# Kernel tuning notes

Hardware: AMD Instinct MI355X
Metric: run time of the kernel (lower is better)

Reference implementation:

```python
import jax, jax.numpy as jnp
import numpy as np

F_REP = 256
F_BET = 512
N_PER = 6
MAGNITUDE = 0.001


def _glorot(key, shape):
    fan_in = shape[0]
    return jax.random.normal(key, shape, dtype=jnp.float32) / np.sqrt(fan_in)


def setup_inputs() -> dict:
    key = jax.random.key(0)
    ks = jax.random.split(key, 24)
    n_atoms, n_tors = 50000, 300000
    inp = {
        'h': jax.random.normal(ks[0], (n_atoms, F_REP), dtype=jnp.float32),
        'idxs': jax.random.randint(ks[1], (n_tors, 4), 0, n_atoms, dtype=jnp.int64),
        # symmetrizer: skippedLinear(4*rep, bet) + DenseBlock(bet, depth=3)
        'Ws0': _glorot(ks[2], (4 * F_REP, F_BET)), 'bs0': jnp.zeros((F_BET,), jnp.float32),
        'Ws1': _glorot(ks[3], (F_BET, F_BET)), 'bs1': jnp.zeros((F_BET,), jnp.float32),
        'Ws2': _glorot(ks[4], (F_BET, F_BET)), 'bs2': jnp.zeros((F_BET,), jnp.float32),
        'Ws3': _glorot(ks[5], (F_BET, F_BET)), 'bs3': jnp.zeros((F_BET,), jnp.float32),
        # torsion_nn: DenseBlock(bet, depth=2) + Linear(bet, n_periodicity)
        'Wt0': _glorot(ks[6], (F_BET, F_BET)), 'bt0': jnp.zeros((F_BET,), jnp.float32),
        'Wt1': _glorot(ks[7], (F_BET, F_BET)), 'bt1': jnp.zeros((F_BET,), jnp.float32),
        'Wt2': _glorot(ks[8], (F_BET, N_PER)), 'bt2': jnp.zeros((N_PER,), jnp.float32),
        # classification_nn: skippedLinear(bet, bet) + Linear(bet, n_periodicity)
        'Wc0': _glorot(ks[9], (F_BET, F_BET)), 'bc0': jnp.zeros((F_BET,), jnp.float32),
        'Wc1': _glorot(ks[10], (F_BET, N_PER)), 'bc1': jnp.zeros((N_PER,), jnp.float32),
    }
    return inp


def _symmetrizer(x, Ws0, bs0, Ws1, bs1, Ws2, bs2, Ws3, bs3):
    # skippedLinear(4*rep, bet): dims differ -> plain Linear + ELU
    h = jax.nn.elu(x @ Ws0 + bs0)
    # DenseBlock: residual Linear+ELU layers (in==out)
    for W, b in ((Ws1, bs1), (Ws2, bs2), (Ws3, bs3)):
        h = h + jax.nn.elu(h @ W + b)
    return h


def reference(h, idxs, Ws0, bs0, Ws1, bs1, Ws2, bs2, Ws3, bs3,
              Wt0, bt0, Wt1, bt1, Wt2, bt2, Wc0, bc0, Wc1, bc1):
    feats = h[idxs]  # [N, 4, F_REP] gather
    f1, f2, f3, f4 = feats[:, 0], feats[:, 1], feats[:, 2], feats[:, 3]
    x_fwd = jnp.concatenate([f1, f2, f3, f4], axis=-1)  # [N, 4F]
    x_rev = jnp.concatenate([f4, f3, f2, f1], axis=-1)
    sym = (_symmetrizer(x_fwd, Ws0, bs0, Ws1, bs1, Ws2, bs2, Ws3, bs3)
           + _symmetrizer(x_rev, Ws0, bs0, Ws1, bs1, Ws2, bs2, Ws3, bs3))
    # torsion_nn
    t = sym + jax.nn.elu(sym @ Wt0 + bt0)
    t = t + jax.nn.elu(t @ Wt1 + bt1)
    coeffs = t @ Wt2 + bt2  # [N, n_periodicity]
    # classification_nn (skippedLinear with in==out -> residual)
    c = sym + jax.nn.elu(sym @ Wc0 + bc0)
    score = c @ Wc1 + bc1  # [N, n_periodicity]
    gate = jax.nn.sigmoid(score)  # hardness == 1
    k = coeffs * MAGNITUDE * gate
    return jnp.stack([score, k])  # [2, N, n_periodicity]
```

## Files before the change

### kernel.cpp

```cpp
#include <hip/hip_runtime.h>

#define BM 64
#define NTHREADS 512
#define BM4 32
#define NT8 512

typedef __attribute__((ext_vector_type(8))) short short8;
typedef __attribute__((ext_vector_type(4))) short short4v;
typedef __attribute__((ext_vector_type(4))) float f32x4;

__device__ __forceinline__ short f2bf(float f) {
  unsigned u = __builtin_bit_cast(unsigned, f);
  u += 0x7FFFu + ((u >> 16) & 1u);
  return (short)(u >> 16);
}
__device__ __forceinline__ float bf2f(short s) {
  unsigned u = ((unsigned)(unsigned short)s) << 16;
  return __builtin_bit_cast(float, u);
}
__device__ __forceinline__ float elu_f(float v) {
  return v > 0.f ? v : (__expf(v) - 1.f);
}
__device__ __forceinline__ unsigned cvt_pk_bf16(float lo, float hi) {
  unsigned r;
  asm("v_cvt_pk_bf16_f32 %0, %1, %2" : "=v"(r) : "v"(lo), "v"(hi));
  return r;
}

__global__ __launch_bounds__(256) void pack_w(const float* __restrict__ src,
                                              short* __restrict__ dst,
                                              int K, int N, int rev) {
  int tile = blockIdx.x * 4 + (threadIdx.x >> 6);
  int lane = threadIdx.x & 63;
  int ktiles = K >> 5;
  int tot = (N >> 4) * ktiles;
  if (tile >= tot) return;
  int nt = tile / ktiles, kt = tile - nt * ktiles;
  int col = (nt << 4) + (lane & 15);
  int k0 = (kt << 5) + ((lane >> 4) << 3);
  short8 o;
#pragma unroll
  for (int j = 0; j < 8; ++j) {
    int kr = k0 + j;
    if (rev) kr = ((3 - (kr >> 8)) << 8) | (kr & 255);
    o[j] = f2bf(src[(size_t)kr * N + col]);
  }
  *(short8*)(dst + (size_t)tile * 512 + lane * 8) = o;
}

__device__ __forceinline__ short8 ldg_bfrag(const short* W, int ktiles, int ct,
                                            int kt, int lane) {
  return *(const short8*)(W + ((size_t)(ct * ktiles + kt) << 9) + (lane << 3));
}

__device__ __forceinline__ int swz(int row, int boff) {
  return row * 1024 + (boff ^ ((row & 7) << 4) ^ (((row >> 3) & 1) << 7));
}
__device__ __forceinline__ short8 lds_act(const char* base, int mt, int kt, int lane) {
  int row = mt * 16 + (lane & 15);
  int boff = (kt << 6) + ((lane >> 4) << 4);
  return *(const short8*)(base + swz(row, boff));
}

__device__ __forceinline__ short8 lds_afrag64(const char* base, int stride, int rt,
                                              int kt, int lane) {
  int row = rt * 16 + (lane & 15);
  int boff = (kt << 6) + ((lane >> 4) << 4);
  return *(const short8*)(base + row * stride + (boff ^ ((row & 7) << 4)));
}

__global__ __launch_bounds__(NTHREADS) void atom_pre(const float* __restrict__ h,
                                                     const short* __restrict__ W0f,
                                                     short* __restrict__ p,
                                                     int n_atoms) {
  __shared__ char sh[BM * 512];
  const int tid = threadIdx.x, lane = tid & 63, wv = tid >> 6;
  const int r0 = blockIdx.x * BM;
  for (int i = tid; i < BM * 32; i += NTHREADS) {
    int row = i >> 5, c0 = (i & 31) << 3;
    int ga = r0 + row;
    short8 o;
    if (ga < n_atoms) {
      const float4* s4 = (const float4*)(h + (size_t)ga * 256 + c0);
      float4 v0 = s4[0], v1 = s4[1];
      o[0] = f2bf(v0.x); o[1] = f2bf(v0.y); o[2] = f2bf(v0.z); o[3] = f2bf(v0.w);
      o[4] = f2bf(v1.x); o[5] = f2bf(v1.y); o[6] = f2bf(v1.z); o[7] = f2bf(v1.w);
    } else {
#pragma unroll
      for (int e = 0; e < 8; ++e) o[e] = 0;
    }
    *(short8*)(sh + row * 512 + ((c0 * 2) ^ ((row & 7) << 4))) = o;
  }
  __syncthreads();
#pragma unroll 1
  for (int s = 0; s < 4; ++s) {
    f32x4 acc[4][4];
    const f32x4 z = {0.f, 0.f, 0.f, 0.f};
#pragma unroll
    for (int rt = 0; rt < 4; ++rt)
#pragma unroll
      for (int cf = 0; cf < 4; ++cf) acc[rt][cf] = z;
    for (int kt = 0; kt < 8; ++kt) {
      short8 a[4], b[4];
#pragma unroll
      for (int rt = 0; rt < 4; ++rt) a[rt] = lds_afrag64(sh, 512, rt, kt, lane);
#pragma unroll
      for (int cf = 0; cf < 4; ++cf)
        b[cf] = ldg_bfrag(W0f, 32, (wv << 2) + cf, (s << 3) + kt, lane);
#pragma unroll
      for (int rt = 0; rt < 4; ++rt)
#pragma unroll
        for (int cf = 0; cf < 4; ++cf)
          acc[rt][cf] = __builtin_amdgcn_mfma_f32_16x16x32_bf16(a[rt], b[cf], acc[rt][cf], 0, 0, 0);
    }
#pragma unroll
    for (int rt = 0; rt < 4; ++rt)
#pragma unroll
      for (int cf = 0; cf < 4; ++cf) {
        int col = (wv << 6) + (cf << 4) + (lane & 15);
#pragma unroll
        for (int i = 0; i < 4; ++i) {
          int row = rt * 16 + ((lane >> 4) << 2) + i;
          int ga = r0 + row;
          if (ga < n_atoms) p[((size_t)ga * 4 + s) * 512 + col] = f2bf(acc[rt][cf][i]);
        }
      }
  }
}

struct P2 {
  const int* idxs;
  const short* p;
  const short *W1, *W2, *W3, *Wt0, *Wt1, *Wc0;
  const float *bs0, *bs1, *bs2, *bs3, *bt0, *bt1, *bt2, *bc0, *bc1;
  const float *Wt2, *Wc1;
  float* out;
  int n_tors;
};


__device__ __forceinline__ void bias_init(const float* __restrict__ bias,
                                          f32x4 (&acc)[2][4], int wv, int lane) {
#pragma unroll
  for (int nf = 0; nf < 4; ++nf) {
    const float4 bv = *(const float4*)(bias + (wv << 6) + (nf << 4) + ((lane >> 4) << 2));
    f32x4 v = {bv.x, bv.y, bv.z, bv.w};
    acc[0][nf] = v;
    acc[1][nf] = v;
  }
}

__device__ __forceinline__ void mfma_dual8(const char* sA, const char* sB,
                                           const short* __restrict__ W,
                                           const float* __restrict__ bias,
                                           f32x4 (&aF)[2][4], f32x4 (&aR)[2][4],
                                           int wv, int lane) {
  bias_init(bias, aF, wv, lane);
  bias_init(bias, aR, wv, lane);
#pragma unroll 4
  for (int kt = 0; kt < 16; ++kt) {
    short8 w[4];
#pragma unroll
    for (int nf = 0; nf < 4; ++nf) w[nf] = ldg_bfrag(W, 16, (wv << 2) + nf, kt, lane);
    short8 bf_[2], br_[2];
#pragma unroll
    for (int mt = 0; mt < 2; ++mt) {
      bf_[mt] = lds_act(sA, mt, kt, lane);
      br_[mt] = lds_act(sB, mt, kt, lane);
    }
#pragma unroll
    for (int mt = 0; mt < 2; ++mt)
#pragma unroll
      for (int nf = 0; nf < 4; ++nf) {
        aF[mt][nf] = __builtin_amdgcn_mfma_f32_16x16x32_bf16(w[nf], bf_[mt], aF[mt][nf], 0, 0, 0);
        aR[mt][nf] = __builtin_amdgcn_mfma_f32_16x16x32_bf16(w[nf], br_[mt], aR[mt][nf], 0, 0, 0);
      }
  }
}

__device__ __forceinline__ void mfma_dualW8(const char* sA,
                                            const short* __restrict__ Wa,
                                            const short* __restrict__ Wb,
                                            const float* __restrict__ ba,
                                            const float* __restrict__ bb,
                                            f32x4 (&aA)[2][4], f32x4 (&aB)[2][4],
                                            int wv, int lane) {
  bias_init(ba, aA, wv, lane);
  bias_init(bb, aB, wv, lane);
#pragma unroll 4
  for (int kt = 0; kt < 16; ++kt) {
    short8 wA[4], wB[4];
#pragma unroll
    for (int nf = 0; nf < 4; ++nf) {
      wA[nf] = ldg_bfrag(Wa, 16, (wv << 2) + nf, kt, lane);
      wB[nf] = ldg_bfrag(Wb, 16, (wv << 2) + nf, kt, lane);
    }
    short8 b[2];
#pragma unroll
    for (int mt = 0; mt < 2; ++mt) b[mt] = lds_act(sA, mt, kt, lane);
#pragma unroll
    for (int mt = 0; mt < 2; ++mt)
#pragma unroll
      for (int nf = 0; nf < 4; ++nf) {
        aA[mt][nf] = __builtin_amdgcn_mfma_f32_16x16x32_bf16(wA[nf], b[mt], aA[mt][nf], 0, 0, 0);
        aB[mt][nf] = __builtin_amdgcn_mfma_f32_16x16x32_bf16(wB[nf], b[mt], aB[mt][nf], 0, 0, 0);
      }
  }
}

__device__ __forceinline__ void mfma_single8(const char* src,
                                             const short* __restrict__ W,
                                             const float* __restrict__ bias,
                                             f32x4 (&acc)[2][4], int wv, int lane) {
  bias_init(bias, acc, wv, lane);
#pragma unroll 4
  for (int kt = 0; kt < 16; ++kt) {
    short8 w[4];
#pragma unroll
    for (int nf = 0; nf < 4; ++nf) w[nf] = ldg_bfrag(W, 16, (wv << 2) + nf, kt, lane);
    short8 b[2];
#pragma unroll
    for (int mt = 0; mt < 2; ++mt) b[mt] = lds_act(src, mt, kt, lane);
#pragma unroll
    for (int mt = 0; mt < 2; ++mt)
#pragma unroll
      for (int nf = 0; nf < 4; ++nf)
        acc[mt][nf] = __builtin_amdgcn_mfma_f32_16x16x32_bf16(w[nf], b[mt], acc[mt][nf], 0, 0, 0);
  }
}

__global__ __launch_bounds__(NT8, 4) void fused9(P2 p) {
  __shared__ char sA[BM4 * 1024];
  __shared__ char sB[BM4 * 1024];
  __shared__ int sIdx[BM4 * 4];
  __shared__ float sSmall[BM4 * 12];
  const int tid = threadIdx.x;
  const int lane = tid & 63;
  const int wv = tid >> 6;
  const int r0 = blockIdx.x * BM4;

  if (tid < BM4 * 4) {
    int grow = r0 + (tid >> 2);
    sIdx[tid] = (grow < p.n_tors) ? p.idxs[(size_t)grow * 4 + (tid & 3)] : 0;
  }
  __syncthreads();

#pragma unroll 1
  for (int i = tid; i < BM4 * 64; i += NT8) {
    int row = i >> 6, c0 = (i & 63) << 3;
    float sf[8], sr[8];
#pragma unroll
    for (int e = 0; e < 8; ++e) { sf[e] = p.bs0[c0 + e]; sr[e] = sf[e]; }
#pragma unroll
    for (int j = 0; j < 4; ++j) {
      int a = sIdx[row * 4 + j];
      short8 vf = *(const short8*)(p.p + ((size_t)a * 4 + j) * 512 + c0);
      short8 vr = *(const short8*)(p.p + ((size_t)a * 4 + (3 - j)) * 512 + c0);
#pragma unroll
      for (int e = 0; e < 8; ++e) { sf[e] += bf2f(vf[e]); sr[e] += bf2f(vr[e]); }
    }
    uint4 of, orv;
    of.x = cvt_pk_bf16(elu_f(sf[0]), elu_f(sf[1]));
    of.y = cvt_pk_bf16(elu_f(sf[2]), elu_f(sf[3]));
    of.z = cvt_pk_bf16(elu_f(sf[4]), elu_f(sf[5]));
    of.w = cvt_pk_bf16(elu_f(sf[6]), elu_f(sf[7]));
    orv.x = cvt_pk_bf16(elu_f(sr[0]), elu_f(sr[1]));
    orv.y = cvt_pk_bf16(elu_f(sr[2]), elu_f(sr[3]));
    orv.z = cvt_pk_bf16(elu_f(sr[4]), elu_f(sr[5]));
    orv.w = cvt_pk_bf16(elu_f(sr[6]), elu_f(sr[7]));
    int off = swz(row, c0 * 2);
    *(uint4*)(sA + off) = of;
    *(uint4*)(sB + off) = orv;
  }
  __syncthreads();

  f32x4 accF[2][4], accR[2][4];

  const short* Ws[3] = {p.W1, p.W2, p.W3};
  const float* bs[3] = {p.bs1, p.bs2, p.bs3};
#pragma unroll 1
  for (int L = 0; L < 3; ++L) {
    mfma_dual8(sA, sB, Ws[L], bs[L], accF, accR, wv, lane);
    __syncthreads();
#pragma unroll
    for (int mt = 0; mt < 2; ++mt)
#pragma unroll
      for (int nf = 0; nf < 4; ++nf) {
        int m = mt * 16 + (lane & 15);
        int nb = ((wv << 6) + (nf << 4) + ((lane >> 4) << 2)) << 1;
        int off = swz(m, nb);
        short4v rf = *(short4v*)(sA + off);
        short4v rr = *(short4v*)(sB + off);
        float vf[4], vr[4];
#pragma unroll
        for (int i = 0; i < 4; ++i) {
          vf[i] = bf2f(rf[i]) + elu_f(accF[mt][nf][i]);
          vr[i] = bf2f(rr[i]) + elu_f(accR[mt][nf][i]);
        }
        if (L == 2) {
          uint2 o;
          o.x = cvt_pk_bf16(vf[0] + vr[0], vf[1] + vr[1]);
          o.y = cvt_pk_bf16(vf[2] + vr[2], vf[3] + vr[3]);
          *(uint2*)(sA + off) = o;
        } else {
          uint2 of, orv;
          of.x = cvt_pk_bf16(vf[0], vf[1]);
          of.y = cvt_pk_bf16(vf[2], vf[3]);
          orv.x = cvt_pk_bf16(vr[0], vr[1]);
          orv.y = cvt_pk_bf16(vr[2], vr[3]);
          *(uint2*)(sA + off) = of;
          *(uint2*)(sB + off) = orv;
        }
      }
    __syncthreads();
  }

  mfma_dualW8(sA, p.Wt0, p.Wc0, p.bt0, p.bc0, accF, accR, wv, lane);
  __syncthreads();
#pragma unroll
  for (int mt = 0; mt < 2; ++mt)
#pragma unroll
    for (int nf = 0; nf < 4; ++nf) {
      int m = mt * 16 + (lane & 15);
      int nb = ((wv << 6) + (nf << 4) + ((lane >> 4) << 2)) << 1;
      int off = swz(m, nb);
      short4v sres = *(short4v*)(sA + off);
      float t0v[4], ccv[4];
#pragma unroll
      for (int i = 0; i < 4; ++i) {
        float s = bf2f(sres[i]);
        t0v[i] = s + elu_f(accF[mt][nf][i]);
        ccv[i] = s + elu_f(accR[mt][nf][i]);
      }
      uint2 t0, cc;
      t0.x = cvt_pk_bf16(t0v[0], t0v[1]);
      t0.y = cvt_pk_bf16(t0v[2], t0v[3]);
      cc.x = cvt_pk_bf16(ccv[0], ccv[1]);
      cc.y = cvt_pk_bf16(ccv[2], ccv[3]);
      *(uint2*)(sB + off) = t0;
      *(uint2*)(sA + off) = cc;
    }
  __syncthreads();

  mfma_single8(sB, p.Wt1, p.bt1, accF, wv, lane);
  __syncthreads();
#pragma unroll
  for (int mt = 0; mt < 2; ++mt)
#pragma unroll
    for (int nf = 0; nf < 4; ++nf) {
      int m = mt * 16 + (lane & 15);
      int nb = ((wv << 6) + (nf << 4) + ((lane >> 4) << 2)) << 1;
      int off = swz(m, nb);
      short4v rt_ = *(short4v*)(sB + off);
      float v[4];
#pragma unroll
      for (int i = 0; i < 4; ++i)
        v[i] = bf2f(rt_[i]) + elu_f(accF[mt][nf][i]);
      uint2 o;
      o.x = cvt_pk_bf16(v[0], v[1]);
      o.y = cvt_pk_bf16(v[2], v[3]);
      *(uint2*)(sB + off) = o;
    }
  __syncthreads();

  if (tid < BM4 * 12) {
    int row = tid / 12, jj = tid - row * 12;
    int j = (jj < 6) ? jj : jj - 6;
    const char* src = (jj < 6) ? sB : sA;
    const float* W = (jj < 6) ? p.Wt2 : p.Wc1;
    float acc = (jj < 6) ? p.bt2[j] : p.bc1[j];
#pragma unroll 1
    for (int c0 = 0; c0 < 512; c0 += 8) {
      short8 v = *(const short8*)(src + swz(row, c0 * 2));
#pragma unroll
      for (int e = 0; e < 8; ++e) acc += bf2f(v[e]) * W[(c0 + e) * 6 + j];
    }
    sSmall[row * 12 + jj] = acc;
  }
  __syncthreads();
  if (tid < BM4 * 6) {
    int row = tid / 6, j = tid - row * 6;
    int grow = r0 + row;
    if (grow < p.n_tors) {
      float score = sSmall[row * 12 + 6 + j];
      float coeff = sSmall[row * 12 + j];
      p.out[(size_t)grow * 6 + j] = score;
      p.out[(size_t)p.n_tors * 6 + (size_t)grow * 6 + j] =
          coeff * 0.001f * (1.0f / (1.0f + __expf(-score)));
    }
  }
}


struct Params {
  const float* h;
  const int* idxs;
  const short *W0f, *W0r, *W1, *W2, *W3, *Wt0, *Wt1, *Wc0;
  const float *bs0, *bs1, *bs2, *bs3, *bt0, *bt1, *bt2, *bc0, *bc1;
  const float *Wt2, *Wc1;
  float* out;
  int n_tors;
};

__device__ __forceinline__ void layer_dual(char* hf, char* hr,
                                           const short* __restrict__ W,
                                           const float* __restrict__ bias,
                                           int wv, int lane) {
  f32x4 accf[4][4], accr[4][4];
  const f32x4 z = {0.f, 0.f, 0.f, 0.f};
#pragma unroll
  for (int rt = 0; rt < 4; ++rt)
#pragma unroll
    for (int cf = 0; cf < 4; ++cf) { accf[rt][cf] = z; accr[rt][cf] = z; }
  for (int kt = 0; kt < 16; ++kt) {
    short8 af[4], ar[4], b[4];
#pragma unroll
    for (int rt = 0; rt < 4; ++rt) {
      af[rt] = lds_afrag64(hf, 1024, rt, kt, lane);
      ar[rt] = lds_afrag64(hr, 1024, rt, kt, lane);
    }
#pragma unroll
    for (int cf = 0; cf < 4; ++cf) b[cf] = ldg_bfrag(W, 16, (wv << 2) + cf, kt, lane);
#pragma unroll
    for (int rt = 0; rt < 4; ++rt)
#pragma unroll
      for (int cf = 0; cf < 4; ++cf) {
        accf[rt][cf] = __builtin_amdgcn_mfma_f32_16x16x32_bf16(af[rt], b[cf], accf[rt][cf], 0, 0, 0);
        accr[rt][cf] = __builtin_amdgcn_mfma_f32_16x16x32_bf16(ar[rt], b[cf], accr[rt][cf], 0, 0, 0);
      }
  }
  float bcol[4];
#pragma unroll
  for (int cf = 0; cf < 4; ++cf) bcol[cf] = bias[(wv << 6) + (cf << 4) + (lane & 15)];
  __syncthreads();
#pragma unroll
  for (int rt = 0; rt < 4; ++rt)
#pragma unroll
    for (int cf = 0; cf < 4; ++cf) {
      int col = (wv << 6) + (cf << 4) + (lane & 15);
#pragma unroll
      for (int i = 0; i < 4; ++i) {
        int row = rt * 16 + ((lane >> 4) << 2) + i;
        size_t off = (size_t)row * 1024 + ((col * 2) ^ ((row & 7) << 4));
        short* pf = (short*)(hf + off);
        short* pr = (short*)(hr + off);
        *pf = f2bf(bf2f(*pf) + elu_f(accf[rt][cf][i] + bcol[cf]));
        *pr = f2bf(bf2f(*pr) + elu_f(accr[rt][cf][i] + bcol[cf]));
      }
    }
  __syncthreads();
}

__device__ __forceinline__ void layer_single(const char* in,
                                             const short* __restrict__ W,
                                             const float* __restrict__ bias,
                                             const char* res, char* out,
                                             int wv, int lane) {
  f32x4 acc[4][4];
  const f32x4 z = {0.f, 0.f, 0.f, 0.f};
#pragma unroll
  for (int rt = 0; rt < 4; ++rt)
#pragma unroll
    for (int cf = 0; cf < 4; ++cf) acc[rt][cf] = z;
  for (int kt = 0; kt < 16; ++kt) {
    short8 a[4], b[4];
#pragma unroll
    for (int rt = 0; rt < 4; ++rt) a[rt] = lds_afrag64(in, 1024, rt, kt, lane);
#pragma unroll
    for (int cf = 0; cf < 4; ++cf) b[cf] = ldg_bfrag(W, 16, (wv << 2) + cf, kt, lane);
#pragma unroll
    for (int rt = 0; rt < 4; ++rt)
#pragma unroll
      for (int cf = 0; cf < 4; ++cf)
        acc[rt][cf] = __builtin_amdgcn_mfma_f32_16x16x32_bf16(a[rt], b[cf], acc[rt][cf], 0, 0, 0);
  }
  float bcol[4];
#pragma unroll
  for (int cf = 0; cf < 4; ++cf) bcol[cf] = bias[(wv << 6) + (cf << 4) + (lane & 15)];
  __syncthreads();
#pragma unroll
  for (int rt = 0; rt < 4; ++rt)
#pragma unroll
    for (int cf = 0; cf < 4; ++cf) {
      int col = (wv << 6) + (cf << 4) + (lane & 15);
#pragma unroll
      for (int i = 0; i < 4; ++i) {
        int row = rt * 16 + ((lane >> 4) << 2) + i;
        size_t off = (size_t)row * 1024 + ((col * 2) ^ ((row & 7) << 4));
        float v = elu_f(acc[rt][cf][i] + bcol[cf]) + bf2f(*(const short*)(res + off));
        *(short*)(out + off) = f2bf(v);
      }
    }
  __syncthreads();
}

__global__ __launch_bounds__(NTHREADS) void fused(Params p) {
  __shared__ char smem[BM * 2048];
  __shared__ float sSmall[BM * 12];
  char* sA = smem;
  char* sB = smem + BM * 1024;
  const int tid = threadIdx.x;
  const int lane = tid & 63;
  const int wv = tid >> 6;
  const int r0 = blockIdx.x * BM;

  for (int c = tid; c < BM * 128; c += NTHREADS) {
    int row = c >> 7;
    int col0 = (c & 127) << 3;
    int grow = r0 + row;
    short8 o;
    if (grow < p.n_tors) {
      int f = col0 >> 8;
      int cin = col0 & 255;
      int a = p.idxs[(size_t)grow * 4 + f];
      const float4* s4 = (const float4*)(p.h + (size_t)a * 256 + cin);
      float4 v0 = s4[0], v1 = s4[1];
      o[0] = f2bf(v0.x); o[1] = f2bf(v0.y); o[2] = f2bf(v0.z); o[3] = f2bf(v0.w);
      o[4] = f2bf(v1.x); o[5] = f2bf(v1.y); o[6] = f2bf(v1.z); o[7] = f2bf(v1.w);
    } else {
#pragma unroll
      for (int e = 0; e < 8; ++e) o[e] = 0;
    }
    *(short8*)(smem + (size_t)row * 2048 + ((col0 * 2) ^ ((row & 7) << 4))) = o;
  }
  __syncthreads();

  {
    f32x4 accf[4][4], accr[4][4];
    const f32x4 z = {0.f, 0.f, 0.f, 0.f};
#pragma unroll
    for (int rt = 0; rt < 4; ++rt)
#pragma unroll
      for (int cf = 0; cf < 4; ++cf) { accf[rt][cf] = z; accr[rt][cf] = z; }
    for (int kt = 0; kt < 32; ++kt) {
      short8 a[4], bfw[4], brw[4];
#pragma unroll
      for (int rt = 0; rt < 4; ++rt) a[rt] = lds_afrag64(smem, 2048, rt, kt, lane);
#pragma unroll
      for (int cf = 0; cf < 4; ++cf) {
        bfw[cf] = ldg_bfrag(p.W0f, 32, (wv << 2) + cf, kt, lane);
        brw[cf] = ldg_bfrag(p.W0r, 32, (wv << 2) + cf, kt, lane);
      }
#pragma unroll
      for (int rt = 0; rt < 4; ++rt)
#pragma unroll
        for (int cf = 0; cf < 4; ++cf) {
          accf[rt][cf] = __builtin_amdgcn_mfma_f32_16x16x32_bf16(a[rt], bfw[cf], accf[rt][cf], 0, 0, 0);
          accr[rt][cf] = __builtin_amdgcn_mfma_f32_16x16x32_bf16(a[rt], brw[cf], accr[rt][cf], 0, 0, 0);
        }
    }
    float bcol[4];
#pragma unroll
    for (int cf = 0; cf < 4; ++cf) bcol[cf] = p.bs0[(wv << 6) + (cf << 4) + (lane & 15)];
    __syncthreads();
#pragma unroll
    for (int rt = 0; rt < 4; ++rt)
#pragma unroll
      for (int cf = 0; cf < 4; ++cf) {
        int col = (wv << 6) + (cf << 4) + (lane & 15);
#pragma unroll
        for (int i = 0; i < 4; ++i) {
          int row = rt * 16 + ((lane >> 4) << 2) + i;
          size_t off = (size_t)row * 1024 + ((col * 2) ^ ((row & 7) << 4));
          *(short*)(sA + off) = f2bf(elu_f(accf[rt][cf][i] + bcol[cf]));
          *(short*)(sB + off) = f2bf(elu_f(accr[rt][cf][i] + bcol[cf]));
        }
      }
    __syncthreads();
  }

  layer_dual(sA, sB, p.W1, p.bs1, wv, lane);
  layer_dual(sA, sB, p.W2, p.bs2, wv, lane);
  layer_dual(sA, sB, p.W3, p.bs3, wv, lane);

  for (int c = tid; c < BM * 64; c += NTHREADS) {
    int row = c >> 6;
    int col0 = (c & 63) << 3;
    size_t off = (size_t)row * 1024 + ((col0 * 2) ^ ((row & 7) << 4));
    short8 xa = *(short8*)(sA + off);
    short8 xb = *(short8*)(sB + off);
    short8 o;
#pragma unroll
    for (int e = 0; e < 8; ++e) o[e] = f2bf(bf2f(xa[e]) + bf2f(xb[e]));
    *(short8*)(sA + off) = o;
  }
  __syncthreads();

  layer_single(sA, p.Wt0, p.bt0, sA, sB, wv, lane);
  layer_single(sB, p.Wt1, p.bt1, sB, sB, wv, lane);
  layer_single(sA, p.Wc0, p.bc0, sA, sA, wv, lane);

  for (int idx = tid; idx < BM * 12; idx += NTHREADS) {
    int row = idx / 12, jj = idx - row * 12;
    int j = (jj < 6) ? jj : jj - 6;
    const char* src = (jj < 6) ? sB : sA;
    const float* W = (jj < 6) ? p.Wt2 : p.Wc1;
    float acc = (jj < 6) ? p.bt2[j] : p.bc1[j];
    for (int c0 = 0; c0 < 512; c0 += 8) {
      short8 v = *(const short8*)(src + (size_t)row * 1024 + ((c0 * 2) ^ ((row & 7) << 4)));
#pragma unroll
      for (int e = 0; e < 8; ++e) acc += bf2f(v[e]) * W[(c0 + e) * 6 + j];
    }
    sSmall[row * 12 + jj] = acc;
  }
  __syncthreads();
  for (int idx = tid; idx < BM * 6; idx += NTHREADS) {
    int row = idx / 6, j = idx - row * 6;
    int grow = r0 + row;
    if (grow < p.n_tors) {
      float score = sSmall[row * 12 + 6 + j];
      float coeff = sSmall[row * 12 + j];
      p.out[(size_t)grow * 6 + j] = score;
      p.out[(size_t)p.n_tors * 6 + (size_t)grow * 6 + j] =
          coeff * 0.001f * (1.0f / (1.0f + __expf(-score)));
    }
  }
}


extern "C" void kernel_launch(void* const* d_in, const int* in_sizes, int n_in,
                              void* d_out, int out_size, void* d_ws, size_t ws_size,
                              hipStream_t stream) {
  const float* h   = (const float*)d_in[0];
  const int* idxs  = (const int*)d_in[1];
  const float* Ws0 = (const float*)d_in[2];
  const float* bs0 = (const float*)d_in[3];
  const float* Ws1 = (const float*)d_in[4];
  const float* bs1 = (const float*)d_in[5];
  const float* Ws2 = (const float*)d_in[6];
  const float* bs2 = (const float*)d_in[7];
  const float* Ws3 = (const float*)d_in[8];
  const float* bs3 = (const float*)d_in[9];
  const float* Wt0 = (const float*)d_in[10];
  const float* bt0 = (const float*)d_in[11];
  const float* Wt1 = (const float*)d_in[12];
  const float* bt1 = (const float*)d_in[13];
  const float* Wt2 = (const float*)d_in[14];
  const float* bt2 = (const float*)d_in[15];
  const float* Wc0 = (const float*)d_in[16];
  const float* bc0 = (const float*)d_in[17];
  const float* Wc1 = (const float*)d_in[18];
  const float* bc1 = (const float*)d_in[19];
  int n_tors = in_sizes[1] / 4;
  int n_atoms = in_sizes[0] / 256;

  auto pk = [&](const float* s, short* dmem, int K, int N, int rev) {
    int tiles = (N >> 4) * (K >> 5);
    pack_w<<<dim3((tiles + 3) / 4), dim3(256), 0, stream>>>(s, dmem, K, N, rev);
  };

  size_t pElems = (size_t)n_atoms * 4 * 512;
  size_t needNew = (pElems + 524288 + 6 * 262144) * sizeof(short);

  if (ws_size >= needNew) {
    short* ws = (short*)d_ws;
    short* pT  = ws;
    short* W0f = ws + pElems;
    short* W1  = W0f + 524288;
    short* W2  = W1 + 262144;
    short* W3  = W2 + 262144;
    short* Wt0c = W3 + 262144;
    short* Wt1c = Wt0c + 262144;
    short* Wc0c = Wt1c + 262144;

    pk(Ws0, W0f, 1024, 512, 0);
    pk(Ws1, W1, 512, 512, 0);
    pk(Ws2, W2, 512, 512, 0);
    pk(Ws3, W3, 512, 512, 0);
    pk(Wt0, Wt0c, 512, 512, 0);
    pk(Wt1, Wt1c, 512, 512, 0);
    pk(Wc0, Wc0c, 512, 512, 0);

    atom_pre<<<dim3((n_atoms + BM - 1) / BM), dim3(NTHREADS), 0, stream>>>(h, W0f, pT, n_atoms);

    P2 p;
    p.idxs = idxs; p.p = pT;
    p.W1 = W1; p.W2 = W2; p.W3 = W3;
    p.Wt0 = Wt0c; p.Wt1 = Wt1c; p.Wc0 = Wc0c;
    p.bs0 = bs0; p.bs1 = bs1; p.bs2 = bs2; p.bs3 = bs3;
    p.bt0 = bt0; p.bt1 = bt1; p.bt2 = bt2; p.bc0 = bc0; p.bc1 = bc1;
    p.Wt2 = Wt2; p.Wc1 = Wc1;
    p.out = (float*)d_out; p.n_tors = n_tors;

    fused9<<<dim3((n_tors + BM4 - 1) / BM4), dim3(NT8), 0, stream>>>(p);
  } else {
    short* ws = (short*)d_ws;
    short* W0f = ws;
    short* W0r = ws + 524288;
    short* W1  = ws + 1048576;
    short* W2  = W1 + 262144;
    short* W3  = W2 + 262144;
    short* Wt0c = W3 + 262144;
    short* Wt1c = Wt0c + 262144;
    short* Wc0c = Wt1c + 262144;

    pk(Ws0, W0f, 1024, 512, 0);
    pk(Ws0, W0r, 1024, 512, 1);
    pk(Ws1, W1, 512, 512, 0);
    pk(Ws2, W2, 512, 512, 0);
    pk(Ws3, W3, 512, 512, 0);
    pk(Wt0, Wt0c, 512, 512, 0);
    pk(Wt1, Wt1c, 512, 512, 0);
    pk(Wc0, Wc0c, 512, 512, 0);

    Params p;
    p.h = h; p.idxs = idxs;
    p.W0f = W0f; p.W0r = W0r; p.W1 = W1; p.W2 = W2; p.W3 = W3;
    p.Wt0 = Wt0c; p.Wt1 = Wt1c; p.Wc0 = Wc0c;
    p.bs0 = bs0; p.bs1 = bs1; p.bs2 = bs2; p.bs3 = bs3;
    p.bt0 = bt0; p.bt1 = bt1; p.bt2 = bt2; p.bc0 = bc0; p.bc1 = bc1;
    p.Wt2 = Wt2; p.Wc1 = Wc1;
    p.out = (float*)d_out; p.n_tors = n_tors;

    fused<<<dim3((n_tors + BM - 1) / BM), dim3(NTHREADS), 0, stream>>>(p);
  }
}
```

Measured before the change: 2.929 ms.

## Double torsion tile to 64 rows with 16 waves per block

The fused torsion MLP kernel now processes 64 torsions per block with 1024 threads (16 waves) instead of 32 torsions with 8 waves. Each wave now covers 32 output columns across 4 row tiles rather than 64 columns across 2 row tiles. This halves the number of blocks, so each weight fragment fetched from global memory feeds more rows. The cost is 128 KB of LDS per block, which limits occupancy, and the k-loops are no longer unrolled, which may expose load latency.

```diff
diff --git a/kernel.cpp b/kernel.cpp
--- a/kernel.cpp
+++ b/kernel.cpp
@@ -2,8 +2,8 @@
 
 #define BM 64
 #define NTHREADS 512
-#define BM4 32
-#define NT8 512
+#define BMX 64
+#define NTX 1024
 
 typedef __attribute__((ext_vector_type(8))) short short8;
 typedef __attribute__((ext_vector_type(4))) short short4v;
@@ -139,114 +139,109 @@
 };
 
 
-__device__ __forceinline__ void bias_init(const float* __restrict__ bias,
-                                          f32x4 (&acc)[2][4], int wv, int lane) {
-#pragma unroll
-  for (int nf = 0; nf < 4; ++nf) {
-    const float4 bv = *(const float4*)(bias + (wv << 6) + (nf << 4) + ((lane >> 4) << 2));
+__device__ __forceinline__ void bias_init10(const float* __restrict__ bias,
+                                            f32x4 (&acc)[4][2], int wv, int lane) {
+#pragma unroll
+  for (int nf = 0; nf < 2; ++nf) {
+    const float4 bv = *(const float4*)(bias + (wv << 5) + (nf << 4) + ((lane >> 4) << 2));
     f32x4 v = {bv.x, bv.y, bv.z, bv.w};
-    acc[0][nf] = v;
-    acc[1][nf] = v;
-  }
-}
-
-__device__ __forceinline__ void mfma_dual8(const char* sA, const char* sB,
-                                           const short* __restrict__ W,
-                                           const float* __restrict__ bias,
-                                           f32x4 (&aF)[2][4], f32x4 (&aR)[2][4],
-                                           int wv, int lane) {
-  bias_init(bias, aF, wv, lane);
-  bias_init(bias, aR, wv, lane);
-#pragma unroll 4
+#pragma unroll
+    for (int mt = 0; mt < 4; ++mt) acc[mt][nf] = v;
+  }
+}
+
+__device__ __forceinline__ void mfma_dual10(const char* sA, const char* sB,
+                                            const short* __restrict__ W,
+                                            const float* __restrict__ bias,
+                                            f32x4 (&aF)[4][2], f32x4 (&aR)[4][2],
+                                            int wv, int lane) {
+  bias_init10(bias, aF, wv, lane);
+  bias_init10(bias, aR, wv, lane);
+#pragma unroll 1
   for (int kt = 0; kt < 16; ++kt) {
-    short8 w[4];
-#pragma unroll
-    for (int nf = 0; nf < 4; ++nf) w[nf] = ldg_bfrag(W, 16, (wv << 2) + nf, kt, lane);
-    short8 bf_[2], br_[2];
-#pragma unroll
-    for (int mt = 0; mt < 2; ++mt) {
-      bf_[mt] = lds_act(sA, mt, kt, lane);
-      br_[mt] = lds_act(sB, mt, kt, lane);
-    }
-#pragma unroll
-    for (int mt = 0; mt < 2; ++mt)
-#pragma unroll
-      for (int nf = 0; nf < 4; ++nf) {
-        aF[mt][nf] = __builtin_amdgcn_mfma_f32_16x16x32_bf16(w[nf], bf_[mt], aF[mt][nf], 0, 0, 0);
-        aR[mt][nf] = __builtin_amdgcn_mfma_f32_16x16x32_bf16(w[nf], br_[mt], aR[mt][nf], 0, 0, 0);
-      }
-  }
-}
-
-__device__ __forceinline__ void mfma_dualW8(const char* sA,
-                                            const short* __restrict__ Wa,
-                                            const short* __restrict__ Wb,
-                                            const float* __restrict__ ba,
-                                            const float* __restrict__ bb,
-                                            f32x4 (&aA)[2][4], f32x4 (&aB)[2][4],
-                                            int wv, int lane) {
-  bias_init(ba, aA, wv, lane);
-  bias_init(bb, aB, wv, lane);
-#pragma unroll 4
+    short8 w[2];
+#pragma unroll
+    for (int nf = 0; nf < 2; ++nf) w[nf] = ldg_bfrag(W, 16, (wv << 1) + nf, kt, lane);
+#pragma unroll
+    for (int mt = 0; mt < 4; ++mt) {
+      short8 bf_ = lds_act(sA, mt, kt, lane);
+      short8 br_ = lds_act(sB, mt, kt, lane);
+#pragma unroll
+      for (int nf = 0; nf < 2; ++nf) {
+        aF[mt][nf] = __builtin_amdgcn_mfma_f32_16x16x32_bf16(w[nf], bf_, aF[mt][nf], 0, 0, 0);
+        aR[mt][nf] = __builtin_amdgcn_mfma_f32_16x16x32_bf16(w[nf], br_, aR[mt][nf], 0, 0, 0);
+      }
+    }
+  }
+}
+
+__device__ __forceinline__ void mfma_dualW10(const char* sA,
+                                             const short* __restrict__ Wa,
+                                             const short* __restrict__ Wb,
+                                             const float* __restrict__ ba,
+                                             const float* __restrict__ bb,
+                                             f32x4 (&aA)[4][2], f32x4 (&aB)[4][2],
+                                             int wv, int lane) {
+  bias_init10(ba, aA, wv, lane);
+  bias_init10(bb, aB, wv, lane);
+#pragma unroll 1
   for (int kt = 0; kt < 16; ++kt) {
-    short8 wA[4], wB[4];
-#pragma unroll
-    for (int nf = 0; nf < 4; ++nf) {
-      wA[nf] = ldg_bfrag(Wa, 16, (wv << 2) + nf, kt, lane);
-      wB[nf] = ldg_bfrag(Wb, 16, (wv << 2) + nf, kt, lane);
-    }
-    short8 b[2];
-#pragma unroll
-    for (int mt = 0; mt < 2; ++mt) b[mt] = lds_act(sA, mt, kt, lane);
-#pragma unroll
-    for (int mt = 0; mt < 2; ++mt)
-#pragma unroll
-      for (int nf = 0; nf < 4; ++nf) {
-        aA[mt][nf] = __builtin_amdgcn_mfma_f32_16x16x32_bf16(wA[nf], b[mt], aA[mt][nf], 0, 0, 0);
-        aB[mt][nf] = __builtin_amdgcn_mfma_f32_16x16x32_bf16(wB[nf], b[mt], aB[mt][nf], 0, 0, 0);
-      }
-  }
-}
-
-__device__ __forceinline__ void mfma_single8(const char* src,
-                                             const short* __restrict__ W,
-                                             const float* __restrict__ bias,
-                                             f32x4 (&acc)[2][4], int wv, int lane) {
-  bias_init(bias, acc, wv, lane);
-#pragma unroll 4
+    short8 wA[2], wB[2];
+#pragma unroll
+    for (int nf = 0; nf < 2; ++nf) {
+      wA[nf] = ldg_bfrag(Wa, 16, (wv << 1) + nf, kt, lane);
+      wB[nf] = ldg_bfrag(Wb, 16, (wv << 1) + nf, kt, lane);
+    }
+#pragma unroll
+    for (int mt = 0; mt < 4; ++mt) {
+      short8 b = lds_act(sA, mt, kt, lane);
+#pragma unroll
+      for (int nf = 0; nf < 2; ++nf) {
+        aA[mt][nf] = __builtin_amdgcn_mfma_f32_16x16x32_bf16(wA[nf], b, aA[mt][nf], 0, 0, 0);
+        aB[mt][nf] = __builtin_amdgcn_mfma_f32_16x16x32_bf16(wB[nf], b, aB[mt][nf], 0, 0, 0);
+      }
+    }
+  }
+}
+
+__device__ __forceinline__ void mfma_single10(const char* src,
+                                              const short* __restrict__ W,
+                                              const float* __restrict__ bias,
+                                              f32x4 (&acc)[4][2], int wv, int lane) {
+  bias_init10(bias, acc, wv, lane);
+#pragma unroll 1
   for (int kt = 0; kt < 16; ++kt) {
-    short8 w[4];
-#pragma unroll
-    for (int nf = 0; nf < 4; ++nf) w[nf] = ldg_bfrag(W, 16, (wv << 2) + nf, kt, lane);
-    short8 b[2];
-#pragma unroll
-    for (int mt = 0; mt < 2; ++mt) b[mt] = lds_act(src, mt, kt, lane);
-#pragma unroll
-    for (int mt = 0; mt < 2; ++mt)
-#pragma unroll
-      for (int nf = 0; nf < 4; ++nf)
-        acc[mt][nf] = __builtin_amdgcn_mfma_f32_16x16x32_bf16(w[nf], b[mt], acc[mt][nf], 0, 0, 0);
-  }
-}
-
-__global__ __launch_bounds__(NT8, 4) void fused9(P2 p) {
-  __shared__ char sA[BM4 * 1024];
-  __shared__ char sB[BM4 * 1024];
-  __shared__ int sIdx[BM4 * 4];
-  __shared__ float sSmall[BM4 * 12];
+    short8 w[2];
+#pragma unroll
+    for (int nf = 0; nf < 2; ++nf) w[nf] = ldg_bfrag(W, 16, (wv << 1) + nf, kt, lane);
+#pragma unroll
+    for (int mt = 0; mt < 4; ++mt) {
+      short8 b = lds_act(src, mt, kt, lane);
+#pragma unroll
+      for (int nf = 0; nf < 2; ++nf)
+        acc[mt][nf] = __builtin_amdgcn_mfma_f32_16x16x32_bf16(w[nf], b, acc[mt][nf], 0, 0, 0);
+    }
+  }
+}
+
+__global__ __launch_bounds__(NTX, 4) void fused10(P2 p) {
+  __shared__ char sA[BMX * 1024];
+  __shared__ char sB[BMX * 1024];
+  __shared__ int sIdx[BMX * 4];
+  __shared__ float sSmall[BMX * 12];
   const int tid = threadIdx.x;
   const int lane = tid & 63;
   const int wv = tid >> 6;
-  const int r0 = blockIdx.x * BM4;
-
-  if (tid < BM4 * 4) {
+  const int r0 = blockIdx.x * BMX;
+
+  if (tid < BMX * 4) {
     int grow = r0 + (tid >> 2);
     sIdx[tid] = (grow < p.n_tors) ? p.idxs[(size_t)grow * 4 + (tid & 3)] : 0;
   }
   __syncthreads();
 
 #pragma unroll 1
-  for (int i = tid; i < BM4 * 64; i += NT8) {
+  for (int i = tid; i < BMX * 64; i += NTX) {
     int row = i >> 6, c0 = (i & 63) << 3;
     float sf[8], sr[8];
 #pragma unroll
@@ -274,20 +269,20 @@
   }
   __syncthreads();
 
-  f32x4 accF[2][4], accR[2][4];
+  f32x4 accF[4][2], accR[4][2];
 
   const short* Ws[3] = {p.W1, p.W2, p.W3};
   const float* bs[3] = {p.bs1, p.bs2, p.bs3};
 #pragma unroll 1
   for (int L = 0; L < 3; ++L) {
-    mfma_dual8(sA, sB, Ws[L], bs[L], accF, accR, wv, lane);
+    mfma_dual10(sA, sB, Ws[L], bs[L], accF, accR, wv, lane);
     __syncthreads();
 #pragma unroll
-    for (int mt = 0; mt < 2; ++mt)
-#pragma unroll
-      for (int nf = 0; nf < 4; ++nf) {
+    for (int mt = 0; mt < 4; ++mt)
+#pragma unroll
+      for (int nf = 0; nf < 2; ++nf) {
         int m = mt * 16 + (lane & 15);
-        int nb = ((wv << 6) + (nf << 4) + ((lane >> 4) << 2)) << 1;
+        int nb = ((wv << 5) + (nf << 4) + ((lane >> 4) << 2)) << 1;
         int off = swz(m, nb);
         short4v rf = *(short4v*)(sA + off);
         short4v rr = *(short4v*)(sB + off);
@@ -315,14 +310,14 @@
     __syncthreads();
   }
 
-  mfma_dualW8(sA, p.Wt0, p.Wc0, p.bt0, p.bc0, accF, accR, wv, lane);
-  __syncthreads();
-#pragma unroll
-  for (int mt = 0; mt < 2; ++mt)
-#pragma unroll
-    for (int nf = 0; nf < 4; ++nf) {
+  mfma_dualW10(sA, p.Wt0, p.Wc0, p.bt0, p.bc0, accF, accR, wv, lane);
+  __syncthreads();
+#pragma unroll
+  for (int mt = 0; mt < 4; ++mt)
+#pragma unroll
+    for (int nf = 0; nf < 2; ++nf) {
       int m = mt * 16 + (lane & 15);
-      int nb = ((wv << 6) + (nf << 4) + ((lane >> 4) << 2)) << 1;
+      int nb = ((wv << 5) + (nf << 4) + ((lane >> 4) << 2)) << 1;
       int off = swz(m, nb);
       short4v sres = *(short4v*)(sA + off);
       float t0v[4], ccv[4];
@@ -342,14 +337,14 @@
     }
   __syncthreads();
 
-  mfma_single8(sB, p.Wt1, p.bt1, accF, wv, lane);
-  __syncthreads();
-#pragma unroll
-  for (int mt = 0; mt < 2; ++mt)
-#pragma unroll
-    for (int nf = 0; nf < 4; ++nf) {
+  mfma_single10(sB, p.Wt1, p.bt1, accF, wv, lane);
+  __syncthreads();
+#pragma unroll
+  for (int mt = 0; mt < 4; ++mt)
+#pragma unroll
+    for (int nf = 0; nf < 2; ++nf) {
       int m = mt * 16 + (lane & 15);
-      int nb = ((wv << 6) + (nf << 4) + ((lane >> 4) << 2)) << 1;
+      int nb = ((wv << 5) + (nf << 4) + ((lane >> 4) << 2)) << 1;
       int off = swz(m, nb);
       short4v rt_ = *(short4v*)(sB + off);
       float v[4];
@@ -363,7 +358,7 @@
     }
   __syncthreads();
 
-  if (tid < BM4 * 12) {
+  if (tid < BMX * 12) {
     int row = tid / 12, jj = tid - row * 12;
     int j = (jj < 6) ? jj : jj - 6;
     const char* src = (jj < 6) ? sB : sA;
@@ -378,7 +373,7 @@
     sSmall[row * 12 + jj] = acc;
   }
   __syncthreads();
-  if (tid < BM4 * 6) {
+  if (tid < BMX * 6) {
     int row = tid / 6, j = tid - row * 6;
     int grow = r0 + row;
     if (grow < p.n_tors) {
@@ -682,7 +677,7 @@
     p.Wt2 = Wt2; p.Wc1 = Wc1;
     p.out = (float*)d_out; p.n_tors = n_tors;
 
-    fused9<<<dim3((n_tors + BM4 - 1) / BM4), dim3(NT8), 0, stream>>>(p);
+    fused10<<<dim3((n_tors + BMX - 1) / BMX), dim3(NTX), 0, stream>>>(p);
   } else {
     short* ws = (short*)d_ws;
     short* W0f = ws;
```

After: 3.113 ms. +6.3%, slower.
